# Performance work log

Measured on AMD Instinct MI355X. Metric: run time of the kernel, lower is better.

## Reference

```python
import jax, jax.numpy as jnp
import numpy as np

B, T, D, P = 32, 2048, 256, 100000
MAX_SPAN = 16


def setup_inputs() -> dict:
    key = jax.random.key(0)
    k0, k1, k2, k3, k4, k5 = jax.random.split(key, 6)
    token_embs = jax.random.normal(k0, (B, T, D), dtype=jnp.float32)
    p1_span = jax.random.randint(k1, (P,), 1, MAX_SPAN + 1, dtype=jnp.int32)
    p2_span = jax.random.randint(k2, (P,), 1, MAX_SPAN + 1, dtype=jnp.int32)
    p1_start = jax.random.randint(k3, (P,), 0, T - MAX_SPAN, dtype=jnp.int32)
    p2_start = jax.random.randint(k4, (P,), 0, T - MAX_SPAN, dtype=jnp.int32)
    pair_batch = jax.random.randint(k5, (P,), 0, B, dtype=jnp.int32)
    return {
        "token_embs": token_embs,
        "p1_start": p1_start,
        "p1_span": p1_span,
        "p2_start": p2_start,
        "p2_span": p2_span,
        "pair_batch": pair_batch,
    }


def reference(token_embs, p1_start, p1_span, p2_start, p2_span, pair_batch):
    # token_embs: [B, T, D]; per-pair ranges [start, start+span) within batch row pair_batch.
    # Range mean via exclusive prefix sums: mean = (csum[end] - csum[start]) / span.
    b, t, d = token_embs.shape
    csum = jnp.concatenate(
        [jnp.zeros((b, 1, d), token_embs.dtype), jnp.cumsum(token_embs, axis=1)],
        axis=1,
    )  # [B, T+1, D]

    def span_mean(start, span):
        end = start + span
        s = csum[pair_batch, end] - csum[pair_batch, start]  # [P, D]
        return s / span[:, None].astype(token_embs.dtype)

    p1 = span_mean(p1_start, p1_span)
    p2 = span_mean(p2_start, p2_span)
    return jnp.concatenate([p1, p2], axis=-1)  # [P, 2D]
```

## Files before the change

kernel.cpp:

```cpp
#include <hip/hip_runtime.h>


#define PB_B 32
#define PB_T 2048
#define PB_D 256
#define PB_P 100000

typedef float vfloat4 __attribute__((ext_vector_type(4)));

__global__ __launch_bounds__(256) void hist_kernel(
    const int* __restrict__ pair_batch, int* __restrict__ counts)
{
    __shared__ int l_cnt[PB_B];
    if (threadIdx.x < PB_B) l_cnt[threadIdx.x] = 0;
    __syncthreads();
    const int i = blockIdx.x * 256 + threadIdx.x;
    if (i < PB_P) atomicAdd(&l_cnt[pair_batch[i]], 1);
    __syncthreads();
    if (threadIdx.x < PB_B && l_cnt[threadIdx.x] > 0)
        atomicAdd(&counts[threadIdx.x], l_cnt[threadIdx.x]);
}

__global__ void scan_counts_kernel(const int* __restrict__ counts,
                                   int* __restrict__ cursors)
{
    if (threadIdx.x == 0 && blockIdx.x == 0) {
        int run = 0;
        #pragma unroll
        for (int b = 0; b < PB_B; ++b) { cursors[b] = run; run += counts[b]; }
    }
}

__global__ __launch_bounds__(256) void scatter_kernel(
    const int* __restrict__ pair_batch,
    const int* __restrict__ p1_start, const int* __restrict__ p1_span,
    const int* __restrict__ p2_start, const int* __restrict__ p2_span,
    int* __restrict__ cursors, int4* __restrict__ meta)
{
    __shared__ int l_cnt[PB_B];
    __shared__ int l_base[PB_B];
    if (threadIdx.x < PB_B) l_cnt[threadIdx.x] = 0;
    __syncthreads();
    const int i = blockIdx.x * 256 + threadIdx.x;
    int b = 0, lpos = 0;
    const bool valid = (i < PB_P);
    if (valid) { b = pair_batch[i]; lpos = atomicAdd(&l_cnt[b], 1); }
    __syncthreads();
    if (threadIdx.x < PB_B && l_cnt[threadIdx.x] > 0)
        l_base[threadIdx.x] = atomicAdd(&cursors[threadIdx.x], l_cnt[threadIdx.x]);
    __syncthreads();
    if (valid) {
        int4 m;
        m.x = i;
        m.y = p1_span[i] | (p2_span[i] << 8);
        m.z = b * PB_T + p1_start[i];
        m.w = b * PB_T + p2_start[i];
        meta[l_base[b] + lpos] = m;
    }
}

__global__ __launch_bounds__(256) void gather_kernel(
    const float* __restrict__ emb, const int4* __restrict__ meta,
    float* __restrict__ out)
{
    const int pos_block = (blockIdx.x & 7) * (PB_P / 4 / 8) + (blockIdx.x >> 3);
    const int pos  = pos_block * 4 + (threadIdx.x >> 6);
    const int lane = threadIdx.x & 63;

    const int4 m = meta[pos];
    const int n1 = m.y & 0xff;
    const int n2 = m.y >> 8;

    const float4* __restrict__ r1 =
        (const float4*)emb + (long long)m.z * (PB_D / 4) + lane;
    const float4* __restrict__ r2 =
        (const float4*)emb + (long long)m.w * (PB_D / 4) + lane;

    float4 a1 = r1[0];
    float4 a2 = r2[0];
    const int nmax = (n1 > n2) ? n1 : n2;
    for (int t = 1; t < nmax; ++t) {
        if (t < n1) {
            float4 v = r1[t * (PB_D / 4)];
            a1.x += v.x; a1.y += v.y; a1.z += v.z; a1.w += v.w;
        }
        if (t < n2) {
            float4 v = r2[t * (PB_D / 4)];
            a2.x += v.x; a2.y += v.y; a2.z += v.z; a2.w += v.w;
        }
    }

    const float i1 = 1.f / (float)n1;
    const float i2 = 1.f / (float)n2;
    vfloat4 o1 = { a1.x * i1, a1.y * i1, a1.z * i1, a1.w * i1 };
    vfloat4 o2 = { a2.x * i2, a2.y * i2, a2.z * i2, a2.w * i2 };

    vfloat4* o = (vfloat4*)(out + (long long)m.x * (2 * PB_D));
    __builtin_nontemporal_store(o1, o + lane);
    __builtin_nontemporal_store(o2, o + 64 + lane);
}

extern "C" void kernel_launch(void* const* d_in, const int* in_sizes, int n_in,
                              void* d_out, int out_size, void* d_ws, size_t ws_size,
                              hipStream_t stream) {
    const float* token_embs = (const float*)d_in[0];
    const int* p1_start = (const int*)d_in[1];
    const int* p1_span  = (const int*)d_in[2];
    const int* p2_start = (const int*)d_in[3];
    const int* p2_span  = (const int*)d_in[4];
    const int* pair_batch = (const int*)d_in[5];
    float* out = (float*)d_out;

    int4* meta   = (int4*)d_ws;
    int* counts  = (int*)(meta + PB_P);
    int* cursors = counts + PB_B;

    (void)hipMemsetAsync(counts, 0, PB_B * sizeof(int), stream);
    const int hb = (PB_P + 255) / 256;
    hist_kernel<<<hb, 256, 0, stream>>>(pair_batch, counts);
    scan_counts_kernel<<<1, 64, 0, stream>>>(counts, cursors);
    scatter_kernel<<<hb, 256, 0, stream>>>(
        pair_batch, p1_start, p1_span, p2_start, p2_span, cursors, meta);

    gather_kernel<<<PB_P / 4, 256, 0, stream>>>(token_embs, meta, out);
}
```

Measured before the change: 332.7 us.

## Bin spans by 16-row window and compute local prefix sums in LDS

Spans are now binned by (batch, 16-row window of start) rather than by batch alone. Each gather block loads a 31-row window of embeddings into shared memory once and builds a local exclusive prefix sum there. Each span is then answered as a difference of two prefix rows. This replaces up to 16 global row reads per span with one shared tile load that all spans in the window share. In exchange there are per-span global atomics in the histogram and scatter passes, a 32KB LDS tile per block, a single-block scan, and many more gather blocks with uneven work per bin.

Result: faster. 306.1 us (-8.0%).

```diff
diff --git a/kernel.cpp b/kernel.cpp
--- a/kernel.cpp
+++ b/kernel.cpp
@@ -5,99 +5,130 @@
 #define PB_T 2048
 #define PB_D 256
 #define PB_P 100000
+#define NSPAN (2 * PB_P)
+#define NWIN 128
+#define NBIN (PB_B * NWIN)
+#define WROWS 31
 
 typedef float vfloat4 __attribute__((ext_vector_type(4)));
 
 __global__ __launch_bounds__(256) void hist_kernel(
+    const int* __restrict__ p1_start, const int* __restrict__ p2_start,
     const int* __restrict__ pair_batch, int* __restrict__ counts)
 {
-    __shared__ int l_cnt[PB_B];
-    if (threadIdx.x < PB_B) l_cnt[threadIdx.x] = 0;
-    __syncthreads();
     const int i = blockIdx.x * 256 + threadIdx.x;
-    if (i < PB_P) atomicAdd(&l_cnt[pair_batch[i]], 1);
-    __syncthreads();
-    if (threadIdx.x < PB_B && l_cnt[threadIdx.x] > 0)
-        atomicAdd(&counts[threadIdx.x], l_cnt[threadIdx.x]);
+    if (i >= PB_P) return;
+    const int b = pair_batch[i];
+    atomicAdd(&counts[(b << 7) + (p1_start[i] >> 4)], 1);
+    atomicAdd(&counts[(b << 7) + (p2_start[i] >> 4)], 1);
 }
 
-__global__ void scan_counts_kernel(const int* __restrict__ counts,
-                                   int* __restrict__ cursors)
+__global__ __launch_bounds__(256) void scan_bins_kernel(
+    const int* __restrict__ counts, int* __restrict__ bin_base,
+    int* __restrict__ cursors)
 {
-    if (threadIdx.x == 0 && blockIdx.x == 0) {
-        int run = 0;
-        #pragma unroll
-        for (int b = 0; b < PB_B; ++b) { cursors[b] = run; run += counts[b]; }
+    __shared__ int wsum[4];
+    const int t = threadIdx.x;
+    int local[16];
+    int run = 0;
+    #pragma unroll
+    for (int i = 0; i < 16; ++i) { local[i] = counts[t * 16 + i]; run += local[i]; }
+
+    const int lane = t & 63, wv = t >> 6;
+    int incl = run;
+    #pragma unroll
+    for (int off = 1; off < 64; off <<= 1) {
+        int v = __shfl_up(incl, off);
+        if (lane >= off) incl += v;
+    }
+    if (lane == 63) wsum[wv] = incl;
+    __syncthreads();
+    int base = incl - run;
+    for (int i = 0; i < wv; ++i) base += wsum[i];
+
+    int c = base;
+    #pragma unroll
+    for (int i = 0; i < 16; ++i) {
+        bin_base[t * 16 + i] = c;
+        cursors[t * 16 + i] = c;
+        c += local[i];
+    }
+    if (t == 255) bin_base[NBIN] = c;
+}
+
+__global__ __launch_bounds__(256) void scatter_kernel(
+    const int* __restrict__ p1_start, const int* __restrict__ p1_span,
+    const int* __restrict__ p2_start, const int* __restrict__ p2_span,
+    const int* __restrict__ pair_batch,
+    int* __restrict__ cursors, int2* __restrict__ meta)
+{
+    const int i = blockIdx.x * 256 + threadIdx.x;
+    if (i >= PB_P) return;
+    const int b = pair_batch[i];
+    {
+        const int s = p1_start[i];
+        const int pos = atomicAdd(&cursors[(b << 7) + (s >> 4)], 1);
+        meta[pos] = make_int2(2 * i, (b << 11) + s + (p1_span[i] << 16));
+    }
+    {
+        const int s = p2_start[i];
+        const int pos = atomicAdd(&cursors[(b << 7) + (s >> 4)], 1);
+        meta[pos] = make_int2(2 * i + 1, (b << 11) + s + (p2_span[i] << 16));
     }
 }
 
-__global__ __launch_bounds__(256) void scatter_kernel(
-    const int* __restrict__ pair_batch,
-    const int* __restrict__ p1_start, const int* __restrict__ p1_span,
-    const int* __restrict__ p2_start, const int* __restrict__ p2_span,
-    int* __restrict__ cursors, int4* __restrict__ meta)
+__global__ __launch_bounds__(512) void gather_kernel(
+    const float* __restrict__ emb, const int2* __restrict__ meta,
+    const int* __restrict__ bin_base, float* __restrict__ out)
 {
-    __shared__ int l_cnt[PB_B];
-    __shared__ int l_base[PB_B];
-    if (threadIdx.x < PB_B) l_cnt[threadIdx.x] = 0;
-    __syncthreads();
-    const int i = blockIdx.x * 256 + threadIdx.x;
-    int b = 0, lpos = 0;
-    const bool valid = (i < PB_P);
-    if (valid) { b = pair_batch[i]; lpos = atomicAdd(&l_cnt[b], 1); }
-    __syncthreads();
-    if (threadIdx.x < PB_B && l_cnt[threadIdx.x] > 0)
-        l_base[threadIdx.x] = atomicAdd(&cursors[threadIdx.x], l_cnt[threadIdx.x]);
-    __syncthreads();
-    if (valid) {
-        int4 m;
-        m.x = i;
-        m.y = p1_span[i] | (p2_span[i] << 8);
-        m.z = b * PB_T + p1_start[i];
-        m.w = b * PB_T + p2_start[i];
-        meta[l_base[b] + lpos] = m;
-    }
-}
+    __shared__ float cs[32 * PB_D];
 
-__global__ __launch_bounds__(256) void gather_kernel(
-    const float* __restrict__ emb, const int4* __restrict__ meta,
-    float* __restrict__ out)
-{
-    const int pos_block = (blockIdx.x & 7) * (PB_P / 4 / 8) + (blockIdx.x >> 3);
-    const int pos  = pos_block * 4 + (threadIdx.x >> 6);
-    const int lane = threadIdx.x & 63;
+    const int blk  = (blockIdx.x & 7) * (NBIN / 8) + (blockIdx.x >> 3);
+    const int b    = blk >> 7;
+    const int row0 = (blk & 127) << 4;
 
-    const int4 m = meta[pos];
-    const int n1 = m.y & 0xff;
-    const int n2 = m.y >> 8;
-
-    const float4* __restrict__ r1 =
-        (const float4*)emb + (long long)m.z * (PB_D / 4) + lane;
-    const float4* __restrict__ r2 =
-        (const float4*)emb + (long long)m.w * (PB_D / 4) + lane;
-
-    float4 a1 = r1[0];
-    float4 a2 = r2[0];
-    const int nmax = (n1 > n2) ? n1 : n2;
-    for (int t = 1; t < nmax; ++t) {
-        if (t < n1) {
-            float4 v = r1[t * (PB_D / 4)];
-            a1.x += v.x; a1.y += v.y; a1.z += v.z; a1.w += v.w;
-        }
-        if (t < n2) {
-            float4 v = r2[t * (PB_D / 4)];
-            a2.x += v.x; a2.y += v.y; a2.z += v.z; a2.w += v.w;
+    const float4* __restrict__ g =
+        (const float4*)(emb + (((long long)b << 11) + row0) * PB_D);
+    float4* l4 = (float4*)cs;
+    const int nf4 = WROWS * (PB_D / 4);
+    const int nvalid = (PB_T - row0 < WROWS ? PB_T - row0 : WROWS) * (PB_D / 4);
+    #pragma unroll
+    for (int k = 0; k < 4; ++k) {
+        const int i = k * 512 + threadIdx.x;
+        if (i < nf4) {
+            float4 v = make_float4(0.f, 0.f, 0.f, 0.f);
+            if (i < nvalid) v = g[i];
+            l4[i] = v;
         }
     }
+    __syncthreads();
 
-    const float i1 = 1.f / (float)n1;
-    const float i2 = 1.f / (float)n2;
-    vfloat4 o1 = { a1.x * i1, a1.y * i1, a1.z * i1, a1.w * i1 };
-    vfloat4 o2 = { a2.x * i2, a2.y * i2, a2.z * i2, a2.w * i2 };
+    if (threadIdx.x < PB_D) {
+        const int d = threadIdx.x;
+        float run = 0.f;
+        #pragma unroll
+        for (int r = 0; r < WROWS; ++r) {
+            const float v = cs[r * PB_D + d];
+            cs[r * PB_D + d] = run;
+            run += v;
+        }
+        cs[WROWS * PB_D + d] = run;
+    }
+    __syncthreads();
 
-    vfloat4* o = (vfloat4*)(out + (long long)m.x * (2 * PB_D));
-    __builtin_nontemporal_store(o1, o + lane);
-    __builtin_nontemporal_store(o2, o + 64 + lane);
+    const int s0 = bin_base[blk], s1 = bin_base[blk + 1];
+    const int lane = threadIdx.x & 63, wv = threadIdx.x >> 6;
+    for (int s = s0 + wv; s < s1; s += 8) {
+        const int2 m = meta[s];
+        const int lr = (m.y & 2047) - row0;
+        const int n  = m.y >> 16;
+        const float4 a = ((const float4*)cs)[lr * (PB_D / 4) + lane];
+        const float4 e = ((const float4*)cs)[(lr + n) * (PB_D / 4) + lane];
+        const float inv = 1.f / (float)n;
+        vfloat4 o = { (e.x - a.x) * inv, (e.y - a.y) * inv,
+                      (e.z - a.z) * inv, (e.w - a.w) * inv };
+        __builtin_nontemporal_store(o, (vfloat4*)out + (long long)m.x * 64 + lane);
+    }
 }
 
 extern "C" void kernel_launch(void* const* d_in, const int* in_sizes, int n_in,
@@ -111,16 +142,17 @@
     const int* pair_batch = (const int*)d_in[5];
     float* out = (float*)d_out;
 
-    int4* meta   = (int4*)d_ws;
-    int* counts  = (int*)(meta + PB_P);
-    int* cursors = counts + PB_B;
+    int2* meta   = (int2*)d_ws;
+    int* counts  = (int*)(meta + NSPAN);
+    int* cursors = counts + NBIN;
+    int* bin_base = cursors + NBIN;
 
-    (void)hipMemsetAsync(counts, 0, PB_B * sizeof(int), stream);
+    (void)hipMemsetAsync(counts, 0, NBIN * sizeof(int), stream);
     const int hb = (PB_P + 255) / 256;
-    hist_kernel<<<hb, 256, 0, stream>>>(pair_batch, counts);
-    scan_counts_kernel<<<1, 64, 0, stream>>>(counts, cursors);
+    hist_kernel<<<hb, 256, 0, stream>>>(p1_start, p2_start, pair_batch, counts);
+    scan_bins_kernel<<<1, 256, 0, stream>>>(counts, bin_base, cursors);
     scatter_kernel<<<hb, 256, 0, stream>>>(
-        pair_batch, p1_start, p1_span, p2_start, p2_span, cursors, meta);
+        p1_start, p1_span, p2_start, p2_span, pair_batch, cursors, meta);
 
-    gather_kernel<<<PB_P / 4, 256, 0, stream>>>(token_embs, meta, out);
+    gather_kernel<<<NBIN, 512, 0, stream>>>(token_embs, meta, bin_base, out);
 }
```
